# Performance work log

Hardware: AMD Instinct MI355X
Metric: run time of the kernel (lower is better)

Reference implementation:

```python
import jax, jax.numpy as jnp
import numpy as np
from jax import lax

EPS_LN = 1e-5
EPS_NORM = 1e-12


def _layernorm_c(x, w, b):
    # WithBias LayerNorm over channel dim of NCHW (equivalent to to_3d -> LN(-1) -> to_4d)
    mu = jnp.mean(x, axis=1, keepdims=True)
    var = jnp.mean(jnp.square(x - mu), axis=1, keepdims=True)
    return (x - mu) / jnp.sqrt(var + EPS_LN) * w[None, :, None, None] + b[None, :, None, None]


def _conv1x1(x, w):
    # w: [O, C] ; x: [B, C, H, W]
    return jnp.einsum('oc,bchw->bohw', w, x)


def _dwconv3x3(x, w):
    # w: [C, 1, 3, 3], depthwise, padding=1
    C = x.shape[1]
    return lax.conv_general_dilated(
        x, w, window_strides=(1, 1), padding=((1, 1), (1, 1)),
        dimension_numbers=('NCHW', 'OIHW', 'NCHW'), feature_group_count=C)


def setup_inputs() -> dict:
    key = jax.random.key(0)
    ks = jax.random.split(key, 8)
    B, C, H, W = 4, 384, 128, 128
    n_heads = 8
    s = 1.0 / np.sqrt(C)
    inp = {
        'x': jax.random.normal(ks[0], (B, C, H, W), jnp.float32),
        'wq': jax.random.normal(ks[1], (C, C), jnp.float32) * s,
        'wk': jax.random.normal(ks[2], (C, C), jnp.float32) * s,
        'wv': jax.random.normal(ks[3], (C, C), jnp.float32) * s,
        'dwq': jax.random.normal(ks[4], (C, 1, 3, 3), jnp.float32) * (1.0 / 3.0),
        'dwk': jax.random.normal(ks[5], (C, 1, 3, 3), jnp.float32) * (1.0 / 3.0),
        'dwv': jax.random.normal(ks[6], (C, 1, 3, 3), jnp.float32) * (1.0 / 3.0),
        'scale': jnp.ones((n_heads, 1, 1), jnp.float32),
        'ln1_w': jnp.ones((C,), jnp.float32),
        'ln1_b': jnp.zeros((C,), jnp.float32),
        'ln2_w': jnp.ones((C,), jnp.float32),
        'ln2_b': jnp.zeros((C,), jnp.float32),
    }
    return inp


def reference(x, wq, wk, wv, dwq, dwk, dwv, scale, ln1_w, ln1_b, ln2_w, ln2_b):
    B, C, H, W = x.shape
    n_heads = scale.shape[0]
    d = C // n_heads
    L = H * W

    x_norm = _layernorm_c(x, ln1_w, ln1_b)
    q = _dwconv3x3(_conv1x1(x_norm, wq), dwq)
    k = _dwconv3x3(_conv1x1(x_norm, wk), dwk)
    v = _dwconv3x3(_conv1x1(x_norm, wv), dwv)

    # b (n d) h w -> b n d L
    q = q.reshape(B, n_heads, d, L)
    k = k.reshape(B, n_heads, d, L)
    v = v.reshape(B, n_heads, d, L)

    # L2-normalize over spatial dim (F.normalize, eps=1e-12)
    q = q / jnp.maximum(jnp.linalg.norm(q, axis=-1, keepdims=True), EPS_NORM)
    k = k / jnp.maximum(jnp.linalg.norm(k, axis=-1, keepdims=True), EPS_NORM)

    # channel (transposed) attention: [b, n, d, d]
    attn = jnp.einsum('bndl,bnel->bnde', q, k) * scale[None]
    attn = jax.nn.softmax(attn, axis=-1)
    out = jnp.einsum('bnde,bnel->bndl', attn, v)

    out = out.reshape(B, C, H, W)
    return _layernorm_c(out, ln2_w, ln2_b)
```

## Files before the change

### kernel.cpp

```cpp
#include <hip/hip_runtime.h>
#include <hip/hip_bf16.h>
#include <stdint.h>

#define B_ 4
#define C_ 384
#define H_ 128
#define W_ 128
#define L_ (H_*W_)
#define NH 8
#define DH 48
#define SPLIT 8

typedef __attribute__((ext_vector_type(8))) short bf16x8;
typedef __attribute__((ext_vector_type(4))) float f32x4;
typedef unsigned short u16;
typedef unsigned int u32;

__device__ __forceinline__ float bf2f(u16 v){
  union { float f; u32 u; } x; x.u = ((u32)v) << 16; return x.f;
}
__device__ __forceinline__ u16 f2bf(float f){
  __hip_bfloat16 h = __float2bfloat16(f);
  return *reinterpret_cast<u16*>(&h);
}

#define GLOAD_LDS16(g, l) \
  __builtin_amdgcn_global_load_lds((const __attribute__((address_space(1))) u32*)(g), \
                                   (__attribute__((address_space(3))) u32*)(l), 16, 0, 0)

__global__ __launch_bounds__(256) void k_cvt_w(const float* __restrict__ wq,
                                               const float* __restrict__ wk,
                                               const float* __restrict__ wv,
                                               u16* __restrict__ wc){
  int i = blockIdx.x * 256 + threadIdx.x;
  if (i >= 3*C_*C_) return;
  int m = i / C_;
  int c = i - m*C_;
  const float* src = (m < C_) ? wq : (m < 2*C_) ? wk : wv;
  int mm = (m >= 2*C_) ? m - 2*C_ : (m >= C_) ? m - C_ : m;
  wc[i] = f2bf(src[mm*C_ + c]);
}

__global__ __launch_bounds__(256) void k_ln1(const float* __restrict__ x,
                                             const float* __restrict__ w,
                                             const float* __restrict__ b,
                                             u16* __restrict__ xt){
  const int tid = threadIdx.x;
  const int bb = blockIdx.x >> 8;
  const int l0 = (blockIdx.x & 255) << 6;
  const int pg = tid >> 4;
  const int cg = tid & 15;
  const int c0 = cg * 24;
  const float* xp = x + (size_t)bb*C_*L_ + (size_t)c0*L_ + l0 + pg*4;

  f32x4 vals[24];
  #pragma unroll
  for (int ci = 0; ci < 24; ++ci)
    vals[ci] = *reinterpret_cast<const f32x4*>(xp + (size_t)ci*L_);

  f32x4 s = {0.f,0.f,0.f,0.f}, s2 = {0.f,0.f,0.f,0.f};
  #pragma unroll
  for (int ci = 0; ci < 24; ++ci){ s += vals[ci]; s2 += vals[ci]*vals[ci]; }
  #pragma unroll
  for (int m = 1; m < 16; m <<= 1){
    #pragma unroll
    for (int r = 0; r < 4; ++r){
      s[r]  += __shfl_xor(s[r],  m);
      s2[r] += __shfl_xor(s2[r], m);
    }
  }
  f32x4 mu, rstd;
  #pragma unroll
  for (int r = 0; r < 4; ++r){
    mu[r]   = s[r] * (1.f/C_);
    rstd[r] = rsqrtf(s2[r]*(1.f/C_) - mu[r]*mu[r] + 1e-5f);
  }

  u16* dst = xt + ((size_t)bb*L_ + l0 + pg*4)*C_ + c0;
  #pragma unroll
  for (int j = 0; j < 3; ++j){
    f32x4 w0 = *reinterpret_cast<const f32x4*>(w + c0 + j*8);
    f32x4 w1 = *reinterpret_cast<const f32x4*>(w + c0 + j*8 + 4);
    f32x4 b0 = *reinterpret_cast<const f32x4*>(b + c0 + j*8);
    f32x4 b1 = *reinterpret_cast<const f32x4*>(b + c0 + j*8 + 4);
    #pragma unroll
    for (int pp = 0; pp < 4; ++pp){
      uint4 pk;
      u16* tp = reinterpret_cast<u16*>(&pk);
      #pragma unroll
      for (int e = 0; e < 4; ++e)
        tp[e]   = f2bf((vals[j*8+e][pp]   - mu[pp]) * rstd[pp] * w0[e] + b0[e]);
      #pragma unroll
      for (int e = 0; e < 4; ++e)
        tp[4+e] = f2bf((vals[j*8+4+e][pp] - mu[pp]) * rstd[pp] * w1[e] + b1[e]);
      *reinterpret_cast<uint4*>(dst + (size_t)pp*C_ + j*8) = pk;
    }
  }
}

__global__ __launch_bounds__(256) void k_gemm(const u16* __restrict__ Wc,
                                              const u16* __restrict__ Xt,
                                              u16* __restrict__ qkv){
  __shared__ u16 As[128*32];
  __shared__ u16 Bs[128*32];
  const int tid = threadIdx.x;
  const int wg = (int)blockIdx.x;
  const int lin = (wg & 7) * 576 + (wg >> 3);
  const int bm = lin % 9;
  const int bn = lin / 9;
  const int m0 = bm * 128;
  const int n0 = bn * 128;
  const int w = tid >> 6, lane = tid & 63;
  const int wm = (w >> 1) * 64, wn = (w & 1) * 64;
  const int fr = lane & 15, kqi = lane >> 4;
  const int sslot = kqi ^ ((fr >> 1) & 3);

  f32x4 acc[4][4] = {};

  for (int k0 = 0; k0 < 384; k0 += 32){
    #pragma unroll
    for (int i = 0; i < 2; ++i){
      int idx = i*256 + tid;
      int row = idx >> 2, q = idx & 3;
      int qs = q ^ ((row >> 1) & 3);
      GLOAD_LDS16(Wc + (size_t)(m0+row)*384 + k0 + qs*8, As + idx*8);
      GLOAD_LDS16(Xt + (size_t)(n0+row)*384 + k0 + qs*8, Bs + idx*8);
    }
    __syncthreads();
    bf16x8 af[4], bfm[4];
    #pragma unroll
    for (int i = 0; i < 4; ++i)
      af[i] = *reinterpret_cast<const bf16x8*>(As + (wm + i*16 + fr)*32 + sslot*8);
    #pragma unroll
    for (int j = 0; j < 4; ++j)
      bfm[j] = *reinterpret_cast<const bf16x8*>(Bs + (wn + j*16 + fr)*32 + sslot*8);
    #pragma unroll
    for (int i = 0; i < 4; ++i)
      #pragma unroll
      for (int j = 0; j < 4; ++j)
        acc[i][j] = __builtin_amdgcn_mfma_f32_16x16x32_bf16(af[i], bfm[j], acc[i][j], 0, 0, 0);
    __syncthreads();
  }

  #pragma unroll
  for (int i = 0; i < 4; ++i){
    int mbase = m0 + wm + i*16 + (lane >> 4) * 4;
    #pragma unroll
    for (int j = 0; j < 4; ++j){
      int n = n0 + wn + j*16 + fr;
      int bb = n >> 14, l = n & (L_-1);
      #pragma unroll
      for (int r = 0; r < 4; ++r){
        int m = mbase + r;
        int proj = (m >= 2*C_) ? 2 : (m >= C_) ? 1 : 0;
        int c = m - proj*C_;
        qkv[(((size_t)proj*B_ + bb)*C_ + c)*L_ + l] = f2bf(acc[i][j][r]);
      }
    }
  }
}

__global__ __launch_bounds__(256) void k_dwconv(u16* __restrict__ qkv,
                                                const float* __restrict__ dwq,
                                                const float* __restrict__ dwk,
                                                const float* __restrict__ dwv,
                                                float* __restrict__ sumsq){
  __shared__ u16 pl[128*128];
  int pid = blockIdx.x;
  int t = pid / (B_*C_);
  int bc = pid - t*(B_*C_);
  int c = bc % C_;
  const float* dw = ((t == 0) ? dwq : (t == 1) ? dwk : dwv) + c*9;
  u16* plane = qkv + ((size_t)t*B_*C_ + bc) * L_;
  int tid = threadIdx.x;
  #pragma unroll
  for (int i = 0; i < 8; ++i){
    int idx = i*256 + tid;
    *reinterpret_cast<uint4*>(pl + idx*8) = *reinterpret_cast<const uint4*>(plane + idx*8);
  }
  float wgt[9];
  #pragma unroll
  for (int i = 0; i < 9; ++i) wgt[i] = dw[i];
  __syncthreads();

  const int tx = tid & 15;
  const int ty = tid >> 4;
  const int lane = tid & 63;
  const int y0 = ty*8;

  float rv[3][8], rl[3], rr_[3];
  float ss = 0.f;

  #pragma unroll
  for (int i = 0; i < 10; ++i){
    const int sl = i % 3;
    int r = y0 - 1 + i;
    int rc = (r < 0) ? 0 : (r > 127 ? 127 : r);
    uint4 pk = *reinterpret_cast<const uint4*>(pl + rc*128 + tx*8);
    const u16* e = reinterpret_cast<const u16*>(&pk);
    bool oob = (r < 0) || (r > 127);
    #pragma unroll
    for (int k = 0; k < 8; ++k)
      rv[sl][k] = oob ? 0.f : bf2f(e[k]);
    float lft = __shfl(rv[sl][7], lane - 1);
    float rgt = __shfl(rv[sl][0], lane + 1);
    rl[sl]  = (tx == 0)  ? 0.f : lft;
    rr_[sl] = (tx == 15) ? 0.f : rgt;

    if (i >= 2){
      const int sa = (i-2) % 3, sb = (i-1) % 3, sc = i % 3;
      const int y = i - 2;
      float o[8];
      #pragma unroll
      for (int xx = 0; xx < 8; ++xx){
        float am1 = (xx == 0) ? rl[sa]  : rv[sa][xx-1];
        float ap1 = (xx == 7) ? rr_[sa] : rv[sa][xx+1];
        float bm1 = (xx == 0) ? rl[sb]  : rv[sb][xx-1];
        float bp1 = (xx == 7) ? rr_[sb] : rv[sb][xx+1];
        float cm1 = (xx == 0) ? rl[sc]  : rv[sc][xx-1];
        float cp1 = (xx == 7) ? rr_[sc] : rv[sc][xx+1];
        float a = wgt[0]*am1 + wgt[1]*rv[sa][xx] + wgt[2]*ap1
                + wgt[3]*bm1 + wgt[4]*rv[sb][xx] + wgt[5]*bp1
                + wgt[6]*cm1 + wgt[7]*rv[sc][xx] + wgt[8]*cp1;
        o[xx] = a;
        ss += a * a;
      }
      uint4 st;
      u16* sp = reinterpret_cast<u16*>(&st);
      #pragma unroll
      for (int xx = 0; xx < 8; ++xx) sp[xx] = f2bf(o[xx]);
      *reinterpret_cast<uint4*>(plane + (y0 + y)*128 + tx*8) = st;
    }
  }

  if (t < 2){
    #pragma unroll
    for (int off = 32; off > 0; off >>= 1) ss += __shfl_down(ss, off);
    __shared__ float red[4];
    if ((tid & 63) == 0) red[tid >> 6] = ss;
    __syncthreads();
    if (tid == 0) sumsq[t*(B_*C_) + bc] = red[0] + red[1] + red[2] + red[3];
  }
}

__global__ __launch_bounds__(256) void k_qk(const u16* __restrict__ qkv,
                                            float* __restrict__ Spart){
  int gid = blockIdx.x;
  int s = gid / (B_*NH);
  int bn = gid - s*(B_*NH);
  int b = bn / NH, n = bn - b*NH;
  const u16* qb = qkv + ((size_t)b*C_ + n*DH) * L_;
  const u16* kb = qkv + ((size_t)B_*C_ + (size_t)b*C_ + n*DH) * L_;
  int tid = threadIdx.x, w = tid >> 6, lane = tid & 63;
  int fr = lane & 15, kq = (lane >> 4) * 8;
  int l0 = s * (L_/SPLIT) + w * (L_/SPLIT/4);
  f32x4 acc[3][3] = {};
  for (int kk = 0; kk < 512; kk += 32){
    int koff = l0 + kk + kq;
    bf16x8 af[3], bfm[3];
    #pragma unroll
    for (int i = 0; i < 3; ++i) af[i]  = *reinterpret_cast<const bf16x8*>(qb + (size_t)(i*16+fr)*L_ + koff);
    #pragma unroll
    for (int j = 0; j < 3; ++j) bfm[j] = *reinterpret_cast<const bf16x8*>(kb + (size_t)(j*16+fr)*L_ + koff);
    #pragma unroll
    for (int i = 0; i < 3; ++i)
      #pragma unroll
      for (int j = 0; j < 3; ++j)
        acc[i][j] = __builtin_amdgcn_mfma_f32_16x16x32_bf16(af[i], bfm[j], acc[i][j], 0, 0, 0);
  }
  __shared__ float red[48*48];
  for (int ww = 0; ww < 4; ++ww){
    if (w == ww){
      #pragma unroll
      for (int i = 0; i < 3; ++i)
        #pragma unroll
        for (int j = 0; j < 3; ++j)
          #pragma unroll
          for (int r = 0; r < 4; ++r){
            int row = i*16 + (lane >> 4)*4 + r;
            int col = j*16 + fr;
            if (ww == 0) red[row*48 + col] = acc[i][j][r];
            else         red[row*48 + col] += acc[i][j][r];
          }
    }
    __syncthreads();
  }
  float* dst = Spart + ((size_t)gid) * 2304;
  for (int idx = tid; idx < 2304; idx += 256) dst[idx] = red[idx];
}

__global__ void k_softmax(const float* __restrict__ Spart,
                          const float* __restrict__ sumsq,
                          const float* __restrict__ scale,
                          u16* __restrict__ attn96){
  int bn = blockIdx.x;
  int b = bn / NH, n = bn - b*NH;
  int i = threadIdx.x;
  if (i >= DH) return;
  const float* sq = sumsq + (size_t)b*C_ + n*DH;
  const float* sk = sumsq + (size_t)B_*C_ + (size_t)b*C_ + n*DH;
  float nq = fmaxf(sqrtf(sq[i]), 1e-12f);
  float sc = scale[n];
  float row[48];
  #pragma unroll
  for (int j = 0; j < DH; ++j){
    float acc = 0.f;
    #pragma unroll
    for (int s = 0; s < SPLIT; ++s)
      acc += Spart[((size_t)(s*(B_*NH) + bn))*2304 + i*48 + j];
    float nk = fmaxf(sqrtf(sk[j]), 1e-12f);
    row[j] = acc / (nq * nk) * sc;
  }
  float m = row[0];
  #pragma unroll
  for (int j = 1; j < DH; ++j) m = fmaxf(m, row[j]);
  float sum = 0.f;
  #pragma unroll
  for (int j = 0; j < DH; ++j){ row[j] = __expf(row[j] - m); sum += row[j]; }
  float inv = 1.f / sum;
  u16* dst = attn96 + ((size_t)bn)*DH*96 + i*96;
  #pragma unroll
  for (int j = 0; j < DH; ++j){
    float a = row[j] * inv;
    u16 hi = f2bf(a);
    float lo = a - bf2f(hi);
    dst[j]      = hi;
    dst[48 + j] = f2bf(lo);
  }
}

#define VT_STRIDE 784
__device__ __forceinline__ int vt_off(int p, int ch){
  return p*VT_STRIDE + ((p>>3)<<4) + 2*ch;
}
__global__ __launch_bounds__(256) void k_av_ln2(const u16* __restrict__ qkv,
                                                const u16* __restrict__ attn96,
                                                const float* __restrict__ w2,
                                                const float* __restrict__ b2,
                                                float* __restrict__ out){
  __shared__ u16 vt[(64*VT_STRIDE + 8*16)/2];
  char* vtb = reinterpret_cast<char*>(vt);
  const int tid = threadIdx.x;
  const int bb = blockIdx.x >> 8;
  const int l0 = (blockIdx.x & 255) << 6;
  const u16* vg = qkv + ((size_t)2*B_*C_ + (size_t)bb*C_)*L_ + l0;

  #pragma unroll
  for (int it = 0; it < 6; ++it){
    int idx = it*256 + tid;
    int cp = idx >> 3, g = idx & 7;
    int c = cp*2;
    uint4 p0 = *reinterpret_cast<const uint4*>(vg + (size_t)c*L_ + g*8);
    uint4 p1 = *reinterpret_cast<const uint4*>(vg + (size_t)(c+1)*L_ + g*8);
    const u16* e0 = reinterpret_cast<const u16*>(&p0);
    const u16* e1 = reinterpret_cast<const u16*>(&p1);
    #pragma unroll
    for (int j = 0; j < 8; ++j){
      int p = g*8 + j;
      u32 packed = ((u32)e0[j]) | (((u32)e1[j]) << 16);
      *reinterpret_cast<u32*>(vtb + vt_off(p, c)) = packed;
    }
  }
  __syncthreads();

  const int w = tid >> 6, lane = tid & 63;
  const int fr = lane & 15, kq = (lane >> 4) * 8;
  const int prow = w*16;
  f32x4 acc[24];
  #pragma unroll
  for (int j = 0; j < 24; ++j) acc[j] = (f32x4){0.f,0.f,0.f,0.f};

  const u16* ab = attn96 + ((size_t)bb*NH)*DH*96;
  #pragma unroll
  for (int n = 0; n < NH; ++n){
    bf16x8 af[3];
    #pragma unroll
    for (int s = 0; s < 3; ++s){
      int ep = s*32 + kq;
      int ch = n*DH + (ep >= 48 ? ep - 48 : ep);
      af[s] = *reinterpret_cast<const bf16x8*>(vtb + vt_off(prow + fr, ch));
    }
    #pragma unroll
    for (int jj = 0; jj < 3; ++jj){
      const u16* arow = ab + ((size_t)n*DH + jj*16 + fr)*96;
      #pragma unroll
      for (int s = 0; s < 3; ++s){
        bf16x8 bf = *reinterpret_cast<const bf16x8*>(arow + s*32 + kq);
        acc[n*3+jj] = __builtin_amdgcn_mfma_f32_16x16x32_bf16(af[s], bf, acc[n*3+jj], 0, 0, 0);
      }
    }
  }

  f32x4 s = {0.f,0.f,0.f,0.f}, s2 = {0.f,0.f,0.f,0.f};
  #pragma unroll
  for (int j = 0; j < 24; ++j){ s += acc[j]; s2 += acc[j]*acc[j]; }
  #pragma unroll
  for (int m = 1; m < 16; m <<= 1){
    #pragma unroll
    for (int r = 0; r < 4; ++r){
      s[r]  += __shfl_xor(s[r],  m);
      s2[r] += __shfl_xor(s2[r], m);
    }
  }
  f32x4 mu, rstd;
  #pragma unroll
  for (int r = 0; r < 4; ++r){
    mu[r]   = s[r] * (1.f/C_);
    rstd[r] = rsqrtf(s2[r]*(1.f/C_) - mu[r]*mu[r] + 1e-5f);
  }
  const int pbase = l0 + prow + (lane>>4)*4;
  #pragma unroll
  for (int j = 0; j < 24; ++j){
    int c = j*16 + fr;
    float wc = w2[c], bc = b2[c];
    f32x4 o;
    #pragma unroll
    for (int r = 0; r < 4; ++r)
      o[r] = (acc[j][r] - mu[r]) * rstd[r] * wc + bc;
    *reinterpret_cast<f32x4*>(out + ((size_t)bb*C_ + c)*L_ + pbase) = o;
  }
}

extern "C" void kernel_launch(void* const* d_in, const int* in_sizes, int n_in,
                              void* d_out, int out_size, void* d_ws, size_t ws_size,
                              hipStream_t stream){
  const float* x     = (const float*)d_in[0];
  const float* wq    = (const float*)d_in[1];
  const float* wk    = (const float*)d_in[2];
  const float* wv    = (const float*)d_in[3];
  const float* dwq   = (const float*)d_in[4];
  const float* dwk   = (const float*)d_in[5];
  const float* dwv   = (const float*)d_in[6];
  const float* scale = (const float*)d_in[7];
  const float* ln1w  = (const float*)d_in[8];
  const float* ln1b  = (const float*)d_in[9];
  const float* ln2w  = (const float*)d_in[10];
  const float* ln2b  = (const float*)d_in[11];
  float* out = (float*)d_out;

  char* ws = (char*)d_ws;
  u16*   qkv    = (u16*)ws;
  u16*   xt     = (u16*)(ws + 150994944);
  u16*   wc     = (u16*)(ws + 201326592);
  float* sumsq  = (float*)(ws + 202211328);
  float* Spart  = (float*)(ws + 202223616);
  u16*   attn96 = (u16*)(ws + 204582912);

  k_cvt_w  <<<1728, 256, 0, stream>>>(wq, wk, wv, wc);
  k_ln1    <<<1024, 256, 0, stream>>>(x, ln1w, ln1b, xt);
  k_gemm   <<<9*512, 256, 0, stream>>>(wc, xt, qkv);
  k_dwconv <<<3*B_*C_, 256, 0, stream>>>(qkv, dwq, dwk, dwv, sumsq);
  k_qk     <<<SPLIT*B_*NH, 256, 0, stream>>>(qkv, Spart);
  k_softmax<<<B_*NH, 64, 0, stream>>>(Spart, sumsq, scale, attn96);
  k_av_ln2 <<<1024, 256, 0, stream>>>(qkv, attn96, ln2w, ln2b, out);
}
```

Measured before the change: 273.6 us.

## Triple-buffer LDS tiles in QKV GEMM with async prefetch two stages ahead

The QKV projection GEMM now keeps three LDS slots for the A and B tiles and issues global-to-LDS loads two k-steps ahead. Each iteration waits with a partial vmcnt and a single barrier, replacing the load/sync/compute/sync pattern. This is meant to hide global memory latency behind the MFMA work. In exchange it triples LDS use per block, which may lower occupancy, and its correctness depends on the hand-tuned vmcnt counts.

Result: no change. 273.3 us (-0.1%).

```diff
diff --git a/kernel.cpp b/kernel.cpp
--- a/kernel.cpp
+++ b/kernel.cpp
@@ -98,11 +98,12 @@
   }
 }
 
+#define SLOTE (128*32)
 __global__ __launch_bounds__(256) void k_gemm(const u16* __restrict__ Wc,
                                               const u16* __restrict__ Xt,
                                               u16* __restrict__ qkv){
-  __shared__ u16 As[128*32];
-  __shared__ u16 Bs[128*32];
+  __shared__ u16 As[3*SLOTE];
+  __shared__ u16 Bs[3*SLOTE];
   const int tid = threadIdx.x;
   const int wg = (int)blockIdx.x;
   const int lin = (wg & 7) * 576 + (wg >> 3);
@@ -117,30 +118,46 @@
 
   f32x4 acc[4][4] = {};
 
-  for (int k0 = 0; k0 < 384; k0 += 32){
-    #pragma unroll
-    for (int i = 0; i < 2; ++i){
-      int idx = i*256 + tid;
-      int row = idx >> 2, q = idx & 3;
-      int qs = q ^ ((row >> 1) & 3);
-      GLOAD_LDS16(Wc + (size_t)(m0+row)*384 + k0 + qs*8, As + idx*8);
-      GLOAD_LDS16(Xt + (size_t)(n0+row)*384 + k0 + qs*8, Bs + idx*8);
-    }
-    __syncthreads();
+#define STAGE(slot, k0) do { \
+    _Pragma("unroll") \
+    for (int i_ = 0; i_ < 2; ++i_){ \
+      int idx_ = i_*256 + tid; \
+      int row_ = idx_ >> 2, q_ = idx_ & 3; \
+      int qs_ = q_ ^ ((row_ >> 1) & 3); \
+      GLOAD_LDS16(Wc + (size_t)(m0+row_)*384 + (k0) + qs_*8, As + (slot)*SLOTE + idx_*8); \
+      GLOAD_LDS16(Xt + (size_t)(n0+row_)*384 + (k0) + qs_*8, Bs + (slot)*SLOTE + idx_*8); \
+    } } while(0)
+
+  STAGE(0, 0);
+  STAGE(1, 32);
+
+  #pragma unroll
+  for (int it = 0; it < 12; ++it){
+    const int cur = it % 3;
+    __builtin_amdgcn_sched_barrier(0);
+    if (it < 11) asm volatile("s_waitcnt vmcnt(4)" ::: "memory");
+    else         asm volatile("s_waitcnt vmcnt(0)" ::: "memory");
+    __builtin_amdgcn_sched_barrier(0);
+    __builtin_amdgcn_s_barrier();
+    __builtin_amdgcn_sched_barrier(0);
+    if (it + 2 < 12) STAGE((it+2)%3, (it+2)*32);
+
+    const u16* Ab = As + cur*SLOTE;
+    const u16* Bb = Bs + cur*SLOTE;
     bf16x8 af[4], bfm[4];
     #pragma unroll
     for (int i = 0; i < 4; ++i)
-      af[i] = *reinterpret_cast<const bf16x8*>(As + (wm + i*16 + fr)*32 + sslot*8);
+      af[i] = *reinterpret_cast<const bf16x8*>(Ab + (wm + i*16 + fr)*32 + sslot*8);
     #pragma unroll
     for (int j = 0; j < 4; ++j)
-      bfm[j] = *reinterpret_cast<const bf16x8*>(Bs + (wn + j*16 + fr)*32 + sslot*8);
+      bfm[j] = *reinterpret_cast<const bf16x8*>(Bb + (wn + j*16 + fr)*32 + sslot*8);
     #pragma unroll
     for (int i = 0; i < 4; ++i)
       #pragma unroll
       for (int j = 0; j < 4; ++j)
         acc[i][j] = __builtin_amdgcn_mfma_f32_16x16x32_bf16(af[i], bfm[j], acc[i][j], 0, 0, 0);
-    __syncthreads();
-  }
+  }
+#undef STAGE
 
   #pragma unroll
   for (int i = 0; i < 4; ++i){
```
